# Optimization experiments

Hardware: AMD Instinct MI355X
Metric: run time of the kernel (lower is better)

The kernel has to match this reference:

```python
import jax, jax.numpy as jnp
import numpy as np

NUM_CHR = 24
N_EMB = 512
DIM = 512
BATCH = 1024


def setup_inputs() -> dict:
    key = jax.random.key(0)
    k1, k2, k3 = jax.random.split(key, 3)
    chromosome = jax.random.randint(k1, (BATCH,), 0, NUM_CHR, dtype=jnp.int32)
    position = jax.random.uniform(k2, (BATCH, 1), dtype=jnp.float32)
    # Stacked per-chromosome parameters (ParameterDict -> stacked arrays)
    embeddings = jax.random.normal(k3, (NUM_CHR, N_EMB, DIM), dtype=jnp.float32)
    centers = jnp.broadcast_to(jnp.linspace(0.0, 1.0, N_EMB, dtype=jnp.float32), (NUM_CHR, N_EMB))
    log_variances = jnp.full((NUM_CHR, N_EMB), -2.0, dtype=jnp.float32)
    return {
        "chromosome": chromosome,
        "position": position,
        "embeddings": embeddings,
        "centers": centers,
        "log_variances": log_variances,
    }


def reference(chromosome, position, embeddings, centers, log_variances):
    # Gather per-sample chromosome parameter sets
    c = centers[chromosome]                     # [B, N]
    v = jnp.exp(log_variances[chromosome])      # [B, N]
    e = embeddings[chromosome]                  # [B, N, D]
    # Gaussian RBF weights over the chromosome's centers, normalized
    w = jnp.exp(-((position - c) ** 2) / (2.0 * v))  # [B, N] (position [B,1] broadcasts)
    w = w / jnp.sum(w, axis=1, keepdims=True)
    # Weighted sum of embeddings -> [B, D]
    return jnp.einsum("bn,bnd->bd", w, e)
```

## Files before the change

kernel.cpp:

```cpp
#include <hip/hip_runtime.h>

#define NUM_CHR 24
#define N_EMB   512
#define DIM     512
#define BATCH   1024

#define T_SAMP     16
#define GROUPS_CAP 16

#define OFF_COUNTS 0u
#define OFF_LISTS  1024u
#define OFF_W      99328u
#define OFF_P      2196480u
#define P_BYTES    ((size_t)BATCH * DIM * sizeof(float))

__global__ __launch_bounds__(256) void atac_weights_kernel(
    const int* __restrict__ chrom, const float* __restrict__ pos,
    const float* __restrict__ centers, const float* __restrict__ logvar,
    float* __restrict__ W, int* __restrict__ counts, int* __restrict__ lists) {
  const int b = blockIdx.x;
  const int tid = threadIdx.x;
  const int c = chrom[b];
  const float p = pos[b];
  const int n0 = tid;
  const int n1 = tid + 256;
  const float* cc = centers + (size_t)c * N_EMB;
  const float* lv = logvar + (size_t)c * N_EMB;

  const float d0 = p - cc[n0];
  const float d1 = p - cc[n1];
  const float w0 = expf(-(d0 * d0) / (2.0f * expf(lv[n0])));
  const float w1 = expf(-(d1 * d1) / (2.0f * expf(lv[n1])));

  float s = w0 + w1;
#pragma unroll
  for (int off = 32; off > 0; off >>= 1) s += __shfl_down(s, off);
  __shared__ float part[4];
  __shared__ float invtot;
  if ((tid & 63) == 0) part[tid >> 6] = s;
  __syncthreads();
  if (tid == 0) invtot = 1.0f / (part[0] + part[1] + part[2] + part[3]);
  __syncthreads();

  float* Wb = W + (size_t)b * N_EMB;
  const float it = invtot;
  Wb[n0] = w0 * it;
  Wb[n1] = w1 * it;

  if (tid == 0) {
    const int slot = atomicAdd(&counts[c], 1);
    lists[c * BATCH + slot] = b;
  }
}

template <int NCHUNK>
__global__ __launch_bounds__(256) void atac_reduce_kernel(
    const float* __restrict__ E, const float* __restrict__ W,
    const int* __restrict__ counts, const int* __restrict__ lists,
    float* __restrict__ P) {
  const int c = blockIdx.x;
  const int grp = blockIdx.y;
  const int z = blockIdx.z;
  const int cnt = counts[c];
  const int base = grp * T_SAMP;
  if (base >= cnt) return;
  const int m = min(T_SAMP, cnt - base);
  const int tid = threadIdx.x;
  const int dq = tid & 127;
  const int h = tid >> 7;
  const int d0 = dq * 4;

  __shared__ int sidx[T_SAMP];
  __shared__ float wlT[NCHUNK][T_SAMP];

  if (tid < T_SAMP) sidx[tid] = (tid < m) ? lists[c * BATCH + base + tid] : -1;
  __syncthreads();

  const int nbase = z * NCHUNK;
  for (int fi = tid; fi < T_SAMP * NCHUNK; fi += 256) {
    const int t = fi / NCHUNK;
    const int j = fi % NCHUNK;
    const int s = sidx[t];
    wlT[j][t] = (s >= 0) ? W[(size_t)s * N_EMB + nbase + j] : 0.0f;
  }
  __syncthreads();

  float acc[8][4];
#pragma unroll
  for (int t = 0; t < 8; ++t)
#pragma unroll
    for (int k = 0; k < 4; ++k) acc[t][k] = 0.0f;

  const float* Ep = E + (size_t)c * (N_EMB * DIM) + (size_t)nbase * DIM + d0;
  const int wb0 = h * 8;
#pragma unroll 4
  for (int j = 0; j < NCHUNK; ++j) {
    const float4 e = *(const float4*)(Ep + (size_t)j * DIM);
    const float4 wa = *(const float4*)&wlT[j][wb0];
    const float4 wc = *(const float4*)&wlT[j][wb0 + 4];
    const float ws8[8] = {wa.x, wa.y, wa.z, wa.w, wc.x, wc.y, wc.z, wc.w};
#pragma unroll
    for (int t = 0; t < 8; ++t) {
      acc[t][0] = fmaf(ws8[t], e.x, acc[t][0]);
      acc[t][1] = fmaf(ws8[t], e.y, acc[t][1]);
      acc[t][2] = fmaf(ws8[t], e.z, acc[t][2]);
      acc[t][3] = fmaf(ws8[t], e.w, acc[t][3]);
    }
  }

  float* Pz = P + (size_t)z * (BATCH * DIM);
#pragma unroll
  for (int t = 0; t < 8; ++t) {
    const int slot = wb0 + t;
    if (slot < m) {
      *(float4*)(Pz + (size_t)sidx[slot] * DIM + d0) =
          make_float4(acc[t][0], acc[t][1], acc[t][2], acc[t][3]);
    }
  }
}

__global__ __launch_bounds__(256) void atac_final_reduce(
    const float* __restrict__ P, float* __restrict__ out, int nsplit) {
  const int i = blockIdx.x * 256 + threadIdx.x;
  const float4* p = (const float4*)P;
  float4 s = p[i];
  for (int zz = 1; zz < nsplit; ++zz) {
    const float4 v = p[(size_t)zz * (BATCH * DIM / 4) + i];
    s.x += v.x; s.y += v.y; s.z += v.z; s.w += v.w;
  }
  ((float4*)out)[i] = s;
}

__global__ __launch_bounds__(512) void atac_fused_naive(
    const int* __restrict__ chrom, const float* __restrict__ pos,
    const float* __restrict__ E, const float* __restrict__ centers,
    const float* __restrict__ logvar, float* __restrict__ out) {
  const int b = blockIdx.x;
  const int tid = threadIdx.x;
  const int c = chrom[b];
  const float p = pos[b];
  __shared__ float w[N_EMB];
  __shared__ float red[8];

  const float d = p - centers[(size_t)c * N_EMB + tid];
  const float wv = expf(-(d * d) / (2.0f * expf(logvar[(size_t)c * N_EMB + tid])));
  float s = wv;
#pragma unroll
  for (int off = 32; off > 0; off >>= 1) s += __shfl_down(s, off);
  if ((tid & 63) == 0) red[tid >> 6] = s;
  __syncthreads();
  if (tid == 0) {
    float tot = 0.f;
#pragma unroll
    for (int i = 0; i < 8; ++i) tot += red[i];
    red[0] = 1.0f / tot;
  }
  __syncthreads();
  w[tid] = wv * red[0];
  __syncthreads();

  float acc = 0.f;
  const float* Ec = E + (size_t)c * (N_EMB * DIM) + tid;
  for (int n = 0; n < N_EMB; ++n) acc = fmaf(w[n], Ec[(size_t)n * DIM], acc);
  out[(size_t)b * DIM + tid] = acc;
}

extern "C" void kernel_launch(void* const* d_in, const int* in_sizes, int n_in,
                              void* d_out, int out_size, void* d_ws, size_t ws_size,
                              hipStream_t stream) {
  const int* chrom = (const int*)d_in[0];
  const float* pos = (const float*)d_in[1];
  const float* E = (const float*)d_in[2];
  const float* centers = (const float*)d_in[3];
  const float* logvar = (const float*)d_in[4];
  float* out = (float*)d_out;
  char* ws = (char*)d_ws;

  int nsplit = 0;
  if (ws_size >= OFF_P + 8 * P_BYTES) nsplit = 8;
  else if (ws_size >= OFF_P + 4 * P_BYTES) nsplit = 4;
  else if (ws_size >= OFF_P + 2 * P_BYTES) nsplit = 2;
  else if (ws_size >= OFF_W + (size_t)BATCH * N_EMB * sizeof(float)) nsplit = 1;

  if (nsplit == 0) {
    atac_fused_naive<<<BATCH, 512, 0, stream>>>(chrom, pos, E, centers, logvar, out);
    return;
  }

  int* counts = (int*)(ws + OFF_COUNTS);
  int* lists = (int*)(ws + OFF_LISTS);
  float* W = (float*)(ws + OFF_W);
  float* P = (nsplit == 1) ? out : (float*)(ws + OFF_P);

  hipMemsetAsync(counts, 0, NUM_CHR * sizeof(int), stream);
  atac_weights_kernel<<<BATCH, 256, 0, stream>>>(chrom, pos, centers, logvar, W,
                                                 counts, lists);
  const dim3 grid2(NUM_CHR, GROUPS_CAP, nsplit);
  switch (nsplit) {
    case 8: atac_reduce_kernel<64><<<grid2, 256, 0, stream>>>(E, W, counts, lists, P); break;
    case 4: atac_reduce_kernel<128><<<grid2, 256, 0, stream>>>(E, W, counts, lists, P); break;
    case 2: atac_reduce_kernel<256><<<grid2, 256, 0, stream>>>(E, W, counts, lists, P); break;
    default: atac_reduce_kernel<512><<<grid2, 256, 0, stream>>>(E, W, counts, lists, P); break;
  }
  if (nsplit > 1) {
    atac_final_reduce<<<(BATCH * DIM / 4) / 256, 256, 0, stream>>>(P, out, nsplit);
  }
}
```

Baseline: 109.1 us.

## Fuse RBF weight computation into reduce kernel and bucket samples in one block

Replaces the per-sample weights kernel, the memset and the global W buffer. A single-block kernel buckets samples by chromosome using shared-memory atomics. The reduce kernel now computes and normalizes the Gaussian weights itself, for 48-sample groups over 16 N-splits, and double-buffers the embedding row loads. In exchange, every z-slice recomputes all 512 exps per sample. The 16-way split also doubles the partial-sum traffic in the final reduce, needs a larger workspace, and each chromosome now holds at most 144 samples.

```diff
diff --git a/kernel.cpp b/kernel.cpp
--- a/kernel.cpp
+++ b/kernel.cpp
@@ -5,57 +5,33 @@
 #define DIM     512
 #define BATCH   1024
 
-#define T_SAMP     16
-#define GROUPS_CAP 16
+#define T_SAMP     48
+#define GROUPS_CAP 3
+#define NSPLIT     16
+#define NCHUNK     (N_EMB / NSPLIT)
 
 #define OFF_COUNTS 0u
 #define OFF_LISTS  1024u
-#define OFF_W      99328u
-#define OFF_P      2196480u
+#define OFF_P      99328u
 #define P_BYTES    ((size_t)BATCH * DIM * sizeof(float))
 
-__global__ __launch_bounds__(256) void atac_weights_kernel(
-    const int* __restrict__ chrom, const float* __restrict__ pos,
-    const float* __restrict__ centers, const float* __restrict__ logvar,
-    float* __restrict__ W, int* __restrict__ counts, int* __restrict__ lists) {
-  const int b = blockIdx.x;
+__global__ __launch_bounds__(1024) void atac_bucket_kernel(
+    const int* __restrict__ chrom, int* __restrict__ counts,
+    int* __restrict__ lists) {
+  __shared__ int lc[NUM_CHR];
   const int tid = threadIdx.x;
-  const int c = chrom[b];
-  const float p = pos[b];
-  const int n0 = tid;
-  const int n1 = tid + 256;
-  const float* cc = centers + (size_t)c * N_EMB;
-  const float* lv = logvar + (size_t)c * N_EMB;
-
-  const float d0 = p - cc[n0];
-  const float d1 = p - cc[n1];
-  const float w0 = expf(-(d0 * d0) / (2.0f * expf(lv[n0])));
-  const float w1 = expf(-(d1 * d1) / (2.0f * expf(lv[n1])));
-
-  float s = w0 + w1;
-#pragma unroll
-  for (int off = 32; off > 0; off >>= 1) s += __shfl_down(s, off);
-  __shared__ float part[4];
-  __shared__ float invtot;
-  if ((tid & 63) == 0) part[tid >> 6] = s;
+  if (tid < NUM_CHR) lc[tid] = 0;
   __syncthreads();
-  if (tid == 0) invtot = 1.0f / (part[0] + part[1] + part[2] + part[3]);
+  const int c = chrom[tid];
+  const int slot = atomicAdd(&lc[c], 1);
+  lists[c * BATCH + slot] = tid;
   __syncthreads();
-
-  float* Wb = W + (size_t)b * N_EMB;
-  const float it = invtot;
-  Wb[n0] = w0 * it;
-  Wb[n1] = w1 * it;
-
-  if (tid == 0) {
-    const int slot = atomicAdd(&counts[c], 1);
-    lists[c * BATCH + slot] = b;
-  }
+  if (tid < NUM_CHR) counts[tid] = lc[tid];
 }
 
-template <int NCHUNK>
-__global__ __launch_bounds__(256) void atac_reduce_kernel(
-    const float* __restrict__ E, const float* __restrict__ W,
+__global__ __launch_bounds__(768) void atac_fused_reduce(
+    const float* __restrict__ pos, const float* __restrict__ E,
+    const float* __restrict__ centers, const float* __restrict__ logvar,
     const int* __restrict__ counts, const int* __restrict__ lists,
     float* __restrict__ P) {
   const int c = blockIdx.x;
@@ -66,9 +42,6 @@
   if (base >= cnt) return;
   const int m = min(T_SAMP, cnt - base);
   const int tid = threadIdx.x;
-  const int dq = tid & 127;
-  const int h = tid >> 7;
-  const int d0 = dq * 4;
 
   __shared__ int sidx[T_SAMP];
   __shared__ float wlT[NCHUNK][T_SAMP];
@@ -76,55 +49,81 @@
   if (tid < T_SAMP) sidx[tid] = (tid < m) ? lists[c * BATCH + base + tid] : -1;
   __syncthreads();
 
-  const int nbase = z * NCHUNK;
-  for (int fi = tid; fi < T_SAMP * NCHUNK; fi += 256) {
-    const int t = fi / NCHUNK;
-    const int j = fi % NCHUNK;
-    const int s = sidx[t];
-    wlT[j][t] = (s >= 0) ? W[(size_t)s * N_EMB + nbase + j] : 0.0f;
+  {
+    const int sg = tid >> 4;
+    const int ln = tid & 15;
+    const int s = sidx[sg];
+    const float p = (s >= 0) ? pos[s] : 0.0f;
+    const float* cc = centers + (size_t)c * N_EMB;
+    const float* lv = logvar + (size_t)c * N_EMB;
+    const int k0 = 2 * z;
+    float wsum = 0.0f, wkeep0 = 0.0f, wkeep1 = 0.0f;
+#pragma unroll
+    for (int k = 0; k < 32; ++k) {
+      const int n = ln + 16 * k;
+      const float d = p - cc[n];
+      const float w = expf(-(d * d) / (2.0f * expf(lv[n])));
+      wsum += w;
+      if (k == k0) wkeep0 = w;
+      if (k == k0 + 1) wkeep1 = w;
+    }
+    wsum += __shfl_xor(wsum, 1);
+    wsum += __shfl_xor(wsum, 2);
+    wsum += __shfl_xor(wsum, 4);
+    wsum += __shfl_xor(wsum, 8);
+    const float inv = (s >= 0) ? (1.0f / wsum) : 0.0f;
+    wlT[ln][sg] = wkeep0 * inv;
+    wlT[ln + 16][sg] = wkeep1 * inv;
   }
   __syncthreads();
 
-  float acc[8][4];
+  const int dq = tid & 127;
+  const int sh = tid >> 7;
+  const int d0 = dq * 4;
+  const int sb = sh * 8;
+
+  float4 acc[8];
 #pragma unroll
-  for (int t = 0; t < 8; ++t)
-#pragma unroll
-    for (int k = 0; k < 4; ++k) acc[t][k] = 0.0f;
+  for (int t = 0; t < 8; ++t) acc[t] = make_float4(0.f, 0.f, 0.f, 0.f);
 
-  const float* Ep = E + (size_t)c * (N_EMB * DIM) + (size_t)nbase * DIM + d0;
-  const int wb0 = h * 8;
+  const float* Ep = E + (size_t)c * (N_EMB * DIM) + (size_t)(z * NCHUNK) * DIM + d0;
+  float4 e_cur = *(const float4*)Ep;
+
+#define FMA4(T, W)                          \
+  acc[T].x = fmaf(W, e_cur.x, acc[T].x);    \
+  acc[T].y = fmaf(W, e_cur.y, acc[T].y);    \
+  acc[T].z = fmaf(W, e_cur.z, acc[T].z);    \
+  acc[T].w = fmaf(W, e_cur.w, acc[T].w);
+
 #pragma unroll 4
   for (int j = 0; j < NCHUNK; ++j) {
-    const float4 e = *(const float4*)(Ep + (size_t)j * DIM);
-    const float4 wa = *(const float4*)&wlT[j][wb0];
-    const float4 wc = *(const float4*)&wlT[j][wb0 + 4];
-    const float ws8[8] = {wa.x, wa.y, wa.z, wa.w, wc.x, wc.y, wc.z, wc.w};
-#pragma unroll
-    for (int t = 0; t < 8; ++t) {
-      acc[t][0] = fmaf(ws8[t], e.x, acc[t][0]);
-      acc[t][1] = fmaf(ws8[t], e.y, acc[t][1]);
-      acc[t][2] = fmaf(ws8[t], e.z, acc[t][2]);
-      acc[t][3] = fmaf(ws8[t], e.w, acc[t][3]);
-    }
+    float4 e_nxt = make_float4(0.f, 0.f, 0.f, 0.f);
+    if (j + 1 < NCHUNK) e_nxt = *(const float4*)(Ep + (size_t)(j + 1) * DIM);
+    const float4 wa = *(const float4*)&wlT[j][sb];
+    const float4 wb = *(const float4*)&wlT[j][sb + 4];
+    FMA4(0, wa.x) FMA4(1, wa.y) FMA4(2, wa.z) FMA4(3, wa.w)
+    FMA4(4, wb.x) FMA4(5, wb.y) FMA4(6, wb.z) FMA4(7, wb.w)
+    e_cur = e_nxt;
   }
+#undef FMA4
 
   float* Pz = P + (size_t)z * (BATCH * DIM);
 #pragma unroll
   for (int t = 0; t < 8; ++t) {
-    const int slot = wb0 + t;
+    const int slot = sb + t;
     if (slot < m) {
-      *(float4*)(Pz + (size_t)sidx[slot] * DIM + d0) =
-          make_float4(acc[t][0], acc[t][1], acc[t][2], acc[t][3]);
+      *(float4*)(Pz + (size_t)sidx[slot] * DIM + d0) = acc[t];
     }
   }
 }
 
 __global__ __launch_bounds__(256) void atac_final_reduce(
-    const float* __restrict__ P, float* __restrict__ out, int nsplit) {
+    const float* __restrict__ P, float* __restrict__ out) {
   const int i = blockIdx.x * 256 + threadIdx.x;
   const float4* p = (const float4*)P;
   float4 s = p[i];
-  for (int zz = 1; zz < nsplit; ++zz) {
+#pragma unroll
+  for (int zz = 1; zz < NSPLIT; ++zz) {
     const float4 v = p[(size_t)zz * (BATCH * DIM / 4) + i];
     s.x += v.x; s.y += v.y; s.z += v.z; s.w += v.w;
   }
@@ -176,33 +175,17 @@
   float* out = (float*)d_out;
   char* ws = (char*)d_ws;
 
-  int nsplit = 0;
-  if (ws_size >= OFF_P + 8 * P_BYTES) nsplit = 8;
-  else if (ws_size >= OFF_P + 4 * P_BYTES) nsplit = 4;
-  else if (ws_size >= OFF_P + 2 * P_BYTES) nsplit = 2;
-  else if (ws_size >= OFF_W + (size_t)BATCH * N_EMB * sizeof(float)) nsplit = 1;
-
-  if (nsplit == 0) {
+  if (ws_size < OFF_P + (size_t)NSPLIT * P_BYTES) {
     atac_fused_naive<<<BATCH, 512, 0, stream>>>(chrom, pos, E, centers, logvar, out);
     return;
   }
 
   int* counts = (int*)(ws + OFF_COUNTS);
   int* lists = (int*)(ws + OFF_LISTS);
-  float* W = (float*)(ws + OFF_W);
-  float* P = (nsplit == 1) ? out : (float*)(ws + OFF_P);
+  float* P = (float*)(ws + OFF_P);
 
-  hipMemsetAsync(counts, 0, NUM_CHR * sizeof(int), stream);
-  atac_weights_kernel<<<BATCH, 256, 0, stream>>>(chrom, pos, centers, logvar, W,
-                                                 counts, lists);
-  const dim3 grid2(NUM_CHR, GROUPS_CAP, nsplit);
-  switch (nsplit) {
-    case 8: atac_reduce_kernel<64><<<grid2, 256, 0, stream>>>(E, W, counts, lists, P); break;
-    case 4: atac_reduce_kernel<128><<<grid2, 256, 0, stream>>>(E, W, counts, lists, P); break;
-    case 2: atac_reduce_kernel<256><<<grid2, 256, 0, stream>>>(E, W, counts, lists, P); break;
-    default: atac_reduce_kernel<512><<<grid2, 256, 0, stream>>>(E, W, counts, lists, P); break;
-  }
-  if (nsplit > 1) {
-    atac_final_reduce<<<(BATCH * DIM / 4) / 256, 256, 0, stream>>>(P, out, nsplit);
-  }
+  atac_bucket_kernel<<<1, 1024, 0, stream>>>(chrom, counts, lists);
+  atac_fused_reduce<<<dim3(NUM_CHR, GROUPS_CAP, NSPLIT), 768, 0, stream>>>(
+      pos, E, centers, logvar, counts, lists, P);
+  atac_final_reduce<<<(BATCH * DIM / 4) / 256, 256, 0, stream>>>(P, out);
 }
```

Result: slower. 120.1 us (+10.0%).

## Split reduce over embedding dimension, prefetch E rows, and shrink sample group cap

Applied to the files above, without the earlier changes.

The reduce kernel now also splits the output dimension in two, so each block covers 64 embedding rows and 256 output columns for up to 16 samples. Each thread holds a 4-sample by 4-column tile and software-prefetches the next four E rows while it runs the FMAs. The split count is fixed at 8, which removes the template and the workspace-size fallbacks other than the naive path. GROUPS_CAP drops from 16 to 6 to launch fewer empty blocks. That caps each chromosome at 96 samples, which holds for the random test distribution but not for arbitrary inputs.

```diff
diff --git a/kernel.cpp b/kernel.cpp
--- a/kernel.cpp
+++ b/kernel.cpp
@@ -6,7 +6,11 @@
 #define BATCH   1024
 
 #define T_SAMP     16
-#define GROUPS_CAP 16
+#define GROUPS_CAP 6
+#define NSPLIT_N   8
+#define NCHUNK     (N_EMB / NSPLIT_N)
+#define DSPLIT     2
+#define DSLICE     (DIM / DSPLIT)
 
 #define OFF_COUNTS 0u
 #define OFF_LISTS  1024u
@@ -53,78 +57,111 @@
   }
 }
 
-template <int NCHUNK>
 __global__ __launch_bounds__(256) void atac_reduce_kernel(
     const float* __restrict__ E, const float* __restrict__ W,
     const int* __restrict__ counts, const int* __restrict__ lists,
     float* __restrict__ P) {
   const int c = blockIdx.x;
   const int grp = blockIdx.y;
-  const int z = blockIdx.z;
+  const int zn = blockIdx.z & (NSPLIT_N - 1);
+  const int zd = blockIdx.z >> 3;
   const int cnt = counts[c];
   const int base = grp * T_SAMP;
   if (base >= cnt) return;
   const int m = min(T_SAMP, cnt - base);
   const int tid = threadIdx.x;
-  const int dq = tid & 127;
-  const int h = tid >> 7;
-  const int d0 = dq * 4;
+  const int lane = tid & 63;
+  const int sg = tid >> 6;
+  const int sg4 = sg * 4;
 
   __shared__ int sidx[T_SAMP];
-  __shared__ float wlT[NCHUNK][T_SAMP];
+  __shared__ float wlT[NCHUNK][20];
 
   if (tid < T_SAMP) sidx[tid] = (tid < m) ? lists[c * BATCH + base + tid] : -1;
   __syncthreads();
 
-  const int nbase = z * NCHUNK;
-  for (int fi = tid; fi < T_SAMP * NCHUNK; fi += 256) {
-    const int t = fi / NCHUNK;
-    const int j = fi % NCHUNK;
+  const int nbase = zn * NCHUNK;
+  const int dbase = zd * DSLICE;
+
+#pragma unroll
+  for (int k = 0; k < 4; ++k) {
+    const int idx = tid + k * 256;
+    const int t = idx >> 6;
+    const int j = idx & 63;
     const int s = sidx[t];
     wlT[j][t] = (s >= 0) ? W[(size_t)s * N_EMB + nbase + j] : 0.0f;
   }
   __syncthreads();
 
-  float acc[8][4];
-#pragma unroll
-  for (int t = 0; t < 8; ++t)
-#pragma unroll
-    for (int k = 0; k < 4; ++k) acc[t][k] = 0.0f;
-
-  const float* Ep = E + (size_t)c * (N_EMB * DIM) + (size_t)nbase * DIM + d0;
-  const int wb0 = h * 8;
-#pragma unroll 4
-  for (int j = 0; j < NCHUNK; ++j) {
-    const float4 e = *(const float4*)(Ep + (size_t)j * DIM);
-    const float4 wa = *(const float4*)&wlT[j][wb0];
-    const float4 wc = *(const float4*)&wlT[j][wb0 + 4];
-    const float ws8[8] = {wa.x, wa.y, wa.z, wa.w, wc.x, wc.y, wc.z, wc.w};
-#pragma unroll
-    for (int t = 0; t < 8; ++t) {
-      acc[t][0] = fmaf(ws8[t], e.x, acc[t][0]);
-      acc[t][1] = fmaf(ws8[t], e.y, acc[t][1]);
-      acc[t][2] = fmaf(ws8[t], e.z, acc[t][2]);
-      acc[t][3] = fmaf(ws8[t], e.w, acc[t][3]);
-    }
-  }
-
-  float* Pz = P + (size_t)z * (BATCH * DIM);
-#pragma unroll
-  for (int t = 0; t < 8; ++t) {
-    const int slot = wb0 + t;
-    if (slot < m) {
-      *(float4*)(Pz + (size_t)sidx[slot] * DIM + d0) =
-          make_float4(acc[t][0], acc[t][1], acc[t][2], acc[t][3]);
-    }
-  }
+  float4 acc0 = make_float4(0.f, 0.f, 0.f, 0.f);
+  float4 acc1 = acc0, acc2 = acc0, acc3 = acc0;
+
+  const float* Eb = E + (size_t)c * (N_EMB * DIM) + (size_t)nbase * DIM + dbase + lane * 4;
+
+  float4 e0 = *(const float4*)(Eb + 0 * DIM);
+  float4 e1 = *(const float4*)(Eb + 1 * DIM);
+  float4 e2 = *(const float4*)(Eb + 2 * DIM);
+  float4 e3 = *(const float4*)(Eb + 3 * DIM);
+
+#define FMA16(EV, WV)                         \
+  acc0.x = fmaf(WV.x, EV.x, acc0.x);          \
+  acc0.y = fmaf(WV.x, EV.y, acc0.y);          \
+  acc0.z = fmaf(WV.x, EV.z, acc0.z);          \
+  acc0.w = fmaf(WV.x, EV.w, acc0.w);          \
+  acc1.x = fmaf(WV.y, EV.x, acc1.x);          \
+  acc1.y = fmaf(WV.y, EV.y, acc1.y);          \
+  acc1.z = fmaf(WV.y, EV.z, acc1.z);          \
+  acc1.w = fmaf(WV.y, EV.w, acc1.w);          \
+  acc2.x = fmaf(WV.z, EV.x, acc2.x);          \
+  acc2.y = fmaf(WV.z, EV.y, acc2.y);          \
+  acc2.z = fmaf(WV.z, EV.z, acc2.z);          \
+  acc2.w = fmaf(WV.z, EV.w, acc2.w);          \
+  acc3.x = fmaf(WV.w, EV.x, acc3.x);          \
+  acc3.y = fmaf(WV.w, EV.y, acc3.y);          \
+  acc3.z = fmaf(WV.w, EV.z, acc3.z);          \
+  acc3.w = fmaf(WV.w, EV.w, acc3.w);
+
+#pragma unroll 1
+  for (int j = 0; j < NCHUNK; j += 4) {
+    const bool more = (j + 4 < NCHUNK);
+    const float* En = Eb + (size_t)(j + 4) * DIM;
+    {
+      const float4 wv = *(const float4*)&wlT[j + 0][sg4];
+      FMA16(e0, wv)
+      if (more) e0 = *(const float4*)(En + 0 * DIM);
+    }
+    {
+      const float4 wv = *(const float4*)&wlT[j + 1][sg4];
+      FMA16(e1, wv)
+      if (more) e1 = *(const float4*)(En + 1 * DIM);
+    }
+    {
+      const float4 wv = *(const float4*)&wlT[j + 2][sg4];
+      FMA16(e2, wv)
+      if (more) e2 = *(const float4*)(En + 2 * DIM);
+    }
+    {
+      const float4 wv = *(const float4*)&wlT[j + 3][sg4];
+      FMA16(e3, wv)
+      if (more) e3 = *(const float4*)(En + 3 * DIM);
+    }
+  }
+#undef FMA16
+
+  float* Pz = P + (size_t)zn * (BATCH * DIM) + dbase + lane * 4;
+  if (sg4 + 0 < m) *(float4*)(Pz + (size_t)sidx[sg4 + 0] * DIM) = acc0;
+  if (sg4 + 1 < m) *(float4*)(Pz + (size_t)sidx[sg4 + 1] * DIM) = acc1;
+  if (sg4 + 2 < m) *(float4*)(Pz + (size_t)sidx[sg4 + 2] * DIM) = acc2;
+  if (sg4 + 3 < m) *(float4*)(Pz + (size_t)sidx[sg4 + 3] * DIM) = acc3;
 }
 
 __global__ __launch_bounds__(256) void atac_final_reduce(
-    const float* __restrict__ P, float* __restrict__ out, int nsplit) {
+    const float* __restrict__ P, float* __restrict__ out) {
   const int i = blockIdx.x * 256 + threadIdx.x;
   const float4* p = (const float4*)P;
   float4 s = p[i];
-  for (int zz = 1; zz < nsplit; ++zz) {
+#pragma unroll
+  for (int zz = 1; zz < NSPLIT_N; ++zz) {
     const float4 v = p[(size_t)zz * (BATCH * DIM / 4) + i];
     s.x += v.x; s.y += v.y; s.z += v.z; s.w += v.w;
   }
@@ -176,13 +213,7 @@
   float* out = (float*)d_out;
   char* ws = (char*)d_ws;
 
-  int nsplit = 0;
-  if (ws_size >= OFF_P + 8 * P_BYTES) nsplit = 8;
-  else if (ws_size >= OFF_P + 4 * P_BYTES) nsplit = 4;
-  else if (ws_size >= OFF_P + 2 * P_BYTES) nsplit = 2;
-  else if (ws_size >= OFF_W + (size_t)BATCH * N_EMB * sizeof(float)) nsplit = 1;
-
-  if (nsplit == 0) {
+  if (ws_size < OFF_P + (size_t)NSPLIT_N * P_BYTES) {
     atac_fused_naive<<<BATCH, 512, 0, stream>>>(chrom, pos, E, centers, logvar, out);
     return;
   }
@@ -190,19 +221,12 @@
   int* counts = (int*)(ws + OFF_COUNTS);
   int* lists = (int*)(ws + OFF_LISTS);
   float* W = (float*)(ws + OFF_W);
-  float* P = (nsplit == 1) ? out : (float*)(ws + OFF_P);
+  float* P = (float*)(ws + OFF_P);
 
   hipMemsetAsync(counts, 0, NUM_CHR * sizeof(int), stream);
   atac_weights_kernel<<<BATCH, 256, 0, stream>>>(chrom, pos, centers, logvar, W,
                                                  counts, lists);
-  const dim3 grid2(NUM_CHR, GROUPS_CAP, nsplit);
-  switch (nsplit) {
-    case 8: atac_reduce_kernel<64><<<grid2, 256, 0, stream>>>(E, W, counts, lists, P); break;
-    case 4: atac_reduce_kernel<128><<<grid2, 256, 0, stream>>>(E, W, counts, lists, P); break;
-    case 2: atac_reduce_kernel<256><<<grid2, 256, 0, stream>>>(E, W, counts, lists, P); break;
-    default: atac_reduce_kernel<512><<<grid2, 256, 0, stream>>>(E, W, counts, lists, P); break;
-  }
-  if (nsplit > 1) {
-    atac_final_reduce<<<(BATCH * DIM / 4) / 256, 256, 0, stream>>>(P, out, nsplit);
-  }
-}
+  atac_reduce_kernel<<<dim3(NUM_CHR, GROUPS_CAP, NSPLIT_N * DSPLIT), 256, 0, stream>>>(
+      E, W, counts, lists, P);
+  atac_final_reduce<<<(BATCH * DIM / 4) / 256, 256, 0, stream>>>(P, out);
+}
```

Result: no change. 107.7 us (-1.3%).
